# Kernel tuning notes

Measured on AMD Instinct MI355X. Metric: run time of the kernel, lower is better.

## Reference

```python
import jax, jax.numpy as jnp
import numpy as np

BATCH = 512          # bs_large + bs_small
COMBINED_BS = 320    # bs_large + bs_small // (r_large // r_small)
R = 64               # r_large
K = 4096             # hidden dim, fixed in the TIR kernel
N_ADAPT = 80         # combined adapters


def setup_inputs() -> dict:
    key = jax.random.key(0)
    k1, k2, k3, k4 = jax.random.split(key, 4)
    x = jax.random.normal(k1, (BATCH, 1, K), dtype=jnp.float32)
    xids = jax.random.randint(k2, (COMBINED_BS * R,), 0, BATCH, dtype=jnp.int32)
    wids = jax.random.randint(k3, (COMBINED_BS,), 0, N_ADAPT, dtype=jnp.int32)
    A = jax.random.normal(k4, (N_ADAPT, K, R), dtype=jnp.float32) * 0.02
    return {"x": x, "xids": xids, "wids": wids, "A": A}


def reference(x, xids, wids, A):
    # out[c, 0, r] = sum_k x[xids[c*R + r], 0, k] * A[wids[c], k, r]
    C = wids.shape[0]
    r = A.shape[2]
    tok = xids.reshape(C, r)          # per-output-element token ids
    xg = x[tok, 0, :]                 # (C, R, K) gathered activations
    Ag = A[wids]                      # (C, K, R) gathered adapters
    out = jnp.einsum('crk,ckr->cr', xg, Ag)
    return out[:, None, :]            # (C, 1, R)
```

## Files before the change

kernel.cpp:

```cpp
#include <hip/hip_runtime.h>
#include <stdint.h>

namespace {
constexpr int BATCH  = 512;
constexpr int CBS    = 320;
constexpr int R      = 64;
constexpr int K      = 4096;
constexpr int NADAPT = 80;
constexpr int SPLIT  = 8;
constexpr int KS     = K / SPLIT;
constexpr int TK     = 64;
constexpr int NT     = 256;
constexpr int NW     = NT / 64;
constexpr int NTILES = KS / TK;

constexpr size_t WS_X_OFF  = 4096;
constexpr size_t WS_NEEDED = WS_X_OFF + (size_t)BATCH * K * 2;

__device__ inline uint16_t f2bf(float f) {
    uint32_t u = __float_as_uint(f);
    u += 0x7fffu + ((u >> 16) & 1u);
    return (uint16_t)(u >> 16);
}
__device__ inline float bf2f(uint16_t b) {
    return __uint_as_float((uint32_t)b << 16);
}
}

__global__ void sort_by_wid(const int* __restrict__ wids, int* __restrict__ perm)
{
    __shared__ int hist[NADAPT];
    __shared__ int offs[NADAPT];
    const int t = threadIdx.x;
    if (t < NADAPT) hist[t] = 0;
    __syncthreads();
    atomicAdd(&hist[wids[t]], 1);
    __syncthreads();
    if (t == 0) {
        int run = 0;
        for (int i = 0; i < NADAPT; ++i) { offs[i] = run; run += hist[i]; }
    }
    __syncthreads();
    const int pos = atomicAdd(&offs[wids[t]], 1);
    perm[pos] = t;
}

__global__ __launch_bounds__(256)
void cvt_x(const float* __restrict__ x, uint16_t* __restrict__ xb)
{
    const int i = blockIdx.x * 256 + threadIdx.x;
    const float4 v = ((const float4*)x)[i];
    ushort4 o;
    o.x = f2bf(v.x); o.y = f2bf(v.y); o.z = f2bf(v.z); o.w = f2bf(v.w);
    ((ushort4*)xb)[i] = o;
}

__global__ __launch_bounds__(NT)
void lora_main(const int* __restrict__ xids,
               const int* __restrict__ wids,
               const float* __restrict__ A,
               const uint16_t* __restrict__ xb,
               const int* __restrict__ perm,
               float* __restrict__ out)
{
    __shared__ float xs[TK * R];
    __shared__ float red[NW * R];

    const int bid  = blockIdx.x;
    const int i0   = bid >> 3;
    const int s    = bid & 7;
    const int c    = perm[i0];
    const int t    = threadIdx.x;
    const int wave = t >> 6;
    const int lane = t & 63;
    const int r4   = lane & 15;
    const int kq   = lane >> 4;

    const int wid = wids[c];
    const float* __restrict__ Aw = A + (size_t)wid * (K * R);

    const int rw  = t >> 2;
    const int jq  = t & 3;
    const int tok = xids[c * R + rw];
    const uint16_t* __restrict__ xrow = xb + (size_t)tok * K + s * KS + jq * 16;
    const int rsw = rw ^ (jq * 16);

    float4 acc = make_float4(0.f, 0.f, 0.f, 0.f);

    uint4 p0, p1;
    {
        const uint4* src = (const uint4*)xrow;
        p0 = src[0]; p1 = src[1];
    }

    for (int tile = 0; tile < NTILES; ++tile) {
        {
            const uint32_t w[8] = {p0.x, p0.y, p0.z, p0.w, p1.x, p1.y, p1.z, p1.w};
            float* base = xs + (jq * 16) * R + rsw;
#pragma unroll
            for (int m = 0; m < 8; ++m) {
                base[(2 * m + 0) * R] = bf2f((uint16_t)(w[m] & 0xffffu));
                base[(2 * m + 1) * R] = bf2f((uint16_t)(w[m] >> 16));
            }
        }
        __syncthreads();

        if (tile + 1 < NTILES) {
            const uint4* src = (const uint4*)(xrow + (tile + 1) * TK);
            p0 = src[0]; p1 = src[1];
        }

        const int kw = wave * 16 + kq;
        const int rr = (4 * r4) ^ (wave * 16);
        const float* __restrict__ Ap =
            Aw + (size_t)(s * KS + tile * TK + kw) * R + 4 * r4;
#pragma unroll
        for (int i = 0; i < 4; ++i) {
            float4 av = *(const float4*)(Ap + (size_t)(4 * i) * R);
            float4 xv = *(const float4*)(&xs[(kw + 4 * i) * R + rr]);
            acc.x = fmaf(xv.x, av.x, acc.x);
            acc.y = fmaf(xv.y, av.y, acc.y);
            acc.z = fmaf(xv.z, av.z, acc.z);
            acc.w = fmaf(xv.w, av.w, acc.w);
        }
        __syncthreads();
    }

#pragma unroll
    for (int m = 16; m < 64; m <<= 1) {
        acc.x += __shfl_xor(acc.x, m, 64);
        acc.y += __shfl_xor(acc.y, m, 64);
        acc.z += __shfl_xor(acc.z, m, 64);
        acc.w += __shfl_xor(acc.w, m, 64);
    }
    if (kq == 0) {
        float* rd = &red[wave * R + 4 * r4];
        rd[0] = acc.x; rd[1] = acc.y; rd[2] = acc.z; rd[3] = acc.w;
    }
    __syncthreads();
    if (wave == 0) {
        float sum = red[lane] + red[R + lane] + red[2 * R + lane] + red[3 * R + lane];
        atomicAdd(&out[c * R + lane], sum);
    }
}

__global__ __launch_bounds__(NT)
void lora_fallback(const float* __restrict__ x,
                   const int*   __restrict__ xids,
                   const int*   __restrict__ wids,
                   const float* __restrict__ A,
                   float*       __restrict__ out)
{
    __shared__ float xs[TK * R];
    __shared__ float red[NW * R];
    const int bid  = blockIdx.x;
    const int c    = bid >> 3;
    const int s    = bid & 7;
    const int t    = threadIdx.x;
    const int wave = t >> 6;
    const int lane = t & 63;
    const int r4   = lane & 15;
    const int kq   = lane >> 4;
    const int wid  = wids[c];
    const float* __restrict__ Aw = A + (size_t)wid * (K * R);
    const int rw  = t >> 2;
    const int jq  = t & 3;
    const int tok = xids[c * R + rw];
    const float* __restrict__ xrow = x + (size_t)tok * K + s * KS + jq * 16;
    float4 acc = make_float4(0.f, 0.f, 0.f, 0.f);
    float4 pv[4];
    {
        const float4* src = (const float4*)xrow;
#pragma unroll
        for (int ii = 0; ii < 4; ++ii) pv[ii] = src[ii];
    }
    for (int tile = 0; tile < NTILES; ++tile) {
#pragma unroll
        for (int ii = 0; ii < 4; ++ii) {
            const int kk = jq * 16 + ii * 4;
            xs[(kk + 0) * R + rw] = pv[ii].x;
            xs[(kk + 1) * R + rw] = pv[ii].y;
            xs[(kk + 2) * R + rw] = pv[ii].z;
            xs[(kk + 3) * R + rw] = pv[ii].w;
        }
        __syncthreads();
        if (tile + 1 < NTILES) {
            const float4* src = (const float4*)(xrow + (tile + 1) * TK);
#pragma unroll
            for (int ii = 0; ii < 4; ++ii) pv[ii] = src[ii];
        }
        const int kw = wave * 16 + kq;
        const float* __restrict__ Ap =
            Aw + (size_t)(s * KS + tile * TK + kw) * R + 4 * r4;
#pragma unroll
        for (int i = 0; i < 4; ++i) {
            float4 av = *(const float4*)(Ap + (size_t)(4 * i) * R);
            float4 xv = *(const float4*)(&xs[(kw + 4 * i) * R + 4 * r4]);
            acc.x = fmaf(xv.x, av.x, acc.x);
            acc.y = fmaf(xv.y, av.y, acc.y);
            acc.z = fmaf(xv.z, av.z, acc.z);
            acc.w = fmaf(xv.w, av.w, acc.w);
        }
        __syncthreads();
    }
#pragma unroll
    for (int m = 16; m < 64; m <<= 1) {
        acc.x += __shfl_xor(acc.x, m, 64);
        acc.y += __shfl_xor(acc.y, m, 64);
        acc.z += __shfl_xor(acc.z, m, 64);
        acc.w += __shfl_xor(acc.w, m, 64);
    }
    if (kq == 0) {
        float* rd = &red[wave * R + 4 * r4];
        rd[0] = acc.x; rd[1] = acc.y; rd[2] = acc.z; rd[3] = acc.w;
    }
    __syncthreads();
    if (wave == 0) {
        float sum = red[lane] + red[R + lane] + red[2 * R + lane] + red[3 * R + lane];
        atomicAdd(&out[c * R + lane], sum);
    }
}

extern "C" void kernel_launch(void* const* d_in, const int* in_sizes, int n_in,
                              void* d_out, int out_size, void* d_ws, size_t ws_size,
                              hipStream_t stream)
{
    (void)in_sizes; (void)n_in;
    const float* x    = (const float*)d_in[0];
    const int*   xids = (const int*)d_in[1];
    const int*   wids = (const int*)d_in[2];
    const float* A    = (const float*)d_in[3];
    float* out        = (float*)d_out;

    hipMemsetAsync(out, 0, (size_t)out_size * sizeof(float), stream);

    if (ws_size >= WS_NEEDED) {
        int*      perm = (int*)d_ws;
        uint16_t* xb   = (uint16_t*)((char*)d_ws + WS_X_OFF);
        hipLaunchKernelGGL(sort_by_wid, dim3(1), dim3(CBS), 0, stream, wids, perm);
        hipLaunchKernelGGL(cvt_x, dim3(BATCH * K / 4 / 256), dim3(256), 0, stream, x, xb);
        hipLaunchKernelGGL(lora_main, dim3(CBS * SPLIT), dim3(NT), 0, stream,
                           xids, wids, A, xb, perm, out);
    } else {
        hipLaunchKernelGGL(lora_fallback, dim3(CBS * SPLIT), dim3(NT), 0, stream,
                           x, xids, wids, A, out);
    }
}
```

Baseline: 147.7 us.

## Group up to four same-adapter rows per block to reuse adapter tile loads

Rows that share an adapter id are bucketed into groups of up to four. Each block now loads one A tile and applies it to up to four gathered activation rows, so A traffic per output row drops. Activations stay packed as bf16 pairs in shared memory and are unpacked at use time. Grid size is now an upper bound on the group count, with empty groups exiting early. In exchange the kernel uses more shared memory and registers per block, and the register prefetch of the next x tile is removed.

```diff
diff --git a/kernel.cpp b/kernel.cpp
--- a/kernel.cpp
+++ b/kernel.cpp
@@ -13,36 +13,45 @@
 constexpr int NT     = 256;
 constexpr int NW     = NT / 64;
 constexpr int NTILES = KS / TK;
-
-constexpr size_t WS_X_OFF  = 4096;
-constexpr size_t WS_NEEDED = WS_X_OFF + (size_t)BATCH * K * 2;
+constexpr int G      = 4;
+constexpr int MAXG   = (CBS + (G - 1) * NADAPT) / G;
+
+constexpr size_t WS_XB_OFF = 8192;
+constexpr size_t WS_NEEDED = WS_XB_OFF + (size_t)BATCH * K * 2;
 
 __device__ inline uint16_t f2bf(float f) {
     uint32_t u = __float_as_uint(f);
     u += 0x7fffu + ((u >> 16) & 1u);
     return (uint16_t)(u >> 16);
 }
-__device__ inline float bf2f(uint16_t b) {
-    return __uint_as_float((uint32_t)b << 16);
-}
-}
-
-__global__ void sort_by_wid(const int* __restrict__ wids, int* __restrict__ perm)
+__device__ inline float bflo(uint32_t u) { return __uint_as_float(u << 16); }
+__device__ inline float bfhi(uint32_t u) { return __uint_as_float(u & 0xffff0000u); }
+}
+
+__global__ void groups_build(const int* __restrict__ wids,
+                             int* __restrict__ gcnt, int* __restrict__ gwid,
+                             int* __restrict__ gc)
 {
     __shared__ int hist[NADAPT];
     __shared__ int offs[NADAPT];
+    __shared__ int gbase[NADAPT];
     const int t = threadIdx.x;
-    if (t < NADAPT) hist[t] = 0;
+    if (t < NADAPT) { hist[t] = 0; offs[t] = 0; }
+    if (t < MAXG) gcnt[t] = 0;
     __syncthreads();
     atomicAdd(&hist[wids[t]], 1);
     __syncthreads();
     if (t == 0) {
         int run = 0;
-        for (int i = 0; i < NADAPT; ++i) { offs[i] = run; run += hist[i]; }
-    }
-    __syncthreads();
-    const int pos = atomicAdd(&offs[wids[t]], 1);
-    perm[pos] = t;
+        for (int w = 0; w < NADAPT; ++w) { gbase[w] = run; run += (hist[w] + G - 1) / G; }
+    }
+    __syncthreads();
+    const int w   = wids[t];
+    const int rk  = atomicAdd(&offs[w], 1);
+    const int gid = gbase[w] + (rk >> 2);
+    gc[gid * G + (rk & 3)] = t;
+    gwid[gid] = w;
+    atomicAdd(&gcnt[gid], 1);
 }
 
 __global__ __launch_bounds__(256)
@@ -57,90 +66,119 @@
 
 __global__ __launch_bounds__(NT)
 void lora_main(const int* __restrict__ xids,
-               const int* __restrict__ wids,
                const float* __restrict__ A,
                const uint16_t* __restrict__ xb,
-               const int* __restrict__ perm,
+               const int* __restrict__ gcnt, const int* __restrict__ gwid,
+               const int* __restrict__ gc,
                float* __restrict__ out)
 {
-    __shared__ float xs[TK * R];
-    __shared__ float red[NW * R];
-
-    const int bid  = blockIdx.x;
-    const int i0   = bid >> 3;
-    const int s    = bid & 7;
-    const int c    = perm[i0];
+    __shared__ uint32_t xs[G * (TK / 2) * R];
+    __shared__ float red[G * NW * R];
+
+    const int bid = blockIdx.x;
+    const int gid = bid >> 3;
+    const int s   = bid & 7;
+    const int cnt = gcnt[gid];
+    if (cnt == 0) return;
+    const int wid = gwid[gid];
+    const float* __restrict__ Aw = A + (size_t)wid * (K * R);
+
     const int t    = threadIdx.x;
     const int wave = t >> 6;
     const int lane = t & 63;
     const int r4   = lane & 15;
     const int kq   = lane >> 4;
-
-    const int wid = wids[c];
-    const float* __restrict__ Aw = A + (size_t)wid * (K * R);
-
-    const int rw  = t >> 2;
-    const int jq  = t & 3;
-    const int tok = xids[c * R + rw];
-    const uint16_t* __restrict__ xrow = xb + (size_t)tok * K + s * KS + jq * 16;
-    const int rsw = rw ^ (jq * 16);
-
-    float4 acc = make_float4(0.f, 0.f, 0.f, 0.f);
-
-    uint4 p0, p1;
+    const int rw   = t >> 2;
+    const int jq   = t & 3;
+    const int rsw  = rw ^ (jq << 4);
+
+    const uint16_t* __restrict__ xrow[G];
+#pragma unroll
+    for (int g = 0; g < G; ++g) {
+        const int c   = (g < cnt) ? gc[gid * G + g] : 0;
+        const int tok = xids[c * R + rw];
+        xrow[g] = xb + (size_t)tok * K + s * KS + jq * 16;
+    }
+
+    float4 acc[G];
+#pragma unroll
+    for (int g = 0; g < G; ++g) acc[g] = make_float4(0.f, 0.f, 0.f, 0.f);
+
+    const int wsw = wave << 4;
+    const int p1  = wave * 8 + kq;
+    const int rr  = (4 * r4) ^ wsw;
+
+    for (int tile = 0; tile < NTILES; ++tile) {
+#pragma unroll
+        for (int g = 0; g < G; ++g) {
+            if (g < cnt) {
+                const uint4* src = (const uint4*)(xrow[g] + tile * TK);
+                uint4 u0 = src[0], u1 = src[1];
+                uint32_t* dst = &xs[g * 2048 + (jq * 8) * R + rsw];
+                dst[0 * R] = u0.x; dst[1 * R] = u0.y; dst[2 * R] = u0.z; dst[3 * R] = u0.w;
+                dst[4 * R] = u1.x; dst[5 * R] = u1.y; dst[6 * R] = u1.z; dst[7 * R] = u1.w;
+            }
+        }
+        __syncthreads();
+
+        const int k0 = s * KS + tile * TK + wave * 16 + 2 * kq;
+        const float* __restrict__ Ap = Aw + (size_t)k0 * R + 4 * r4;
+        const float4 a0 = *(const float4*)(Ap);
+        const float4 a1 = *(const float4*)(Ap + R);
+        const float4 a2 = *(const float4*)(Ap + 8 * R);
+        const float4 a3 = *(const float4*)(Ap + 9 * R);
+
+#pragma unroll
+        for (int g = 0; g < G; ++g) {
+            if (g < cnt) {
+                const uint32_t* b = &xs[g * 2048];
+                const uint4 f1 = *(const uint4*)&b[p1 * R + rr];
+                const uint4 f2 = *(const uint4*)&b[(p1 + 4) * R + rr];
+                acc[g].x = fmaf(bflo(f1.x), a0.x, acc[g].x);
+                acc[g].y = fmaf(bflo(f1.y), a0.y, acc[g].y);
+                acc[g].z = fmaf(bflo(f1.z), a0.z, acc[g].z);
+                acc[g].w = fmaf(bflo(f1.w), a0.w, acc[g].w);
+                acc[g].x = fmaf(bfhi(f1.x), a1.x, acc[g].x);
+                acc[g].y = fmaf(bfhi(f1.y), a1.y, acc[g].y);
+                acc[g].z = fmaf(bfhi(f1.z), a1.z, acc[g].z);
+                acc[g].w = fmaf(bfhi(f1.w), a1.w, acc[g].w);
+                acc[g].x = fmaf(bflo(f2.x), a2.x, acc[g].x);
+                acc[g].y = fmaf(bflo(f2.y), a2.y, acc[g].y);
+                acc[g].z = fmaf(bflo(f2.z), a2.z, acc[g].z);
+                acc[g].w = fmaf(bflo(f2.w), a2.w, acc[g].w);
+                acc[g].x = fmaf(bfhi(f2.x), a3.x, acc[g].x);
+                acc[g].y = fmaf(bfhi(f2.y), a3.y, acc[g].y);
+                acc[g].z = fmaf(bfhi(f2.z), a3.z, acc[g].z);
+                acc[g].w = fmaf(bfhi(f2.w), a3.w, acc[g].w);
+            }
+        }
+        __syncthreads();
+    }
+
+#pragma unroll
+    for (int g = 0; g < G; ++g) {
+#pragma unroll
+        for (int m = 16; m < 64; m <<= 1) {
+            acc[g].x += __shfl_xor(acc[g].x, m, 64);
+            acc[g].y += __shfl_xor(acc[g].y, m, 64);
+            acc[g].z += __shfl_xor(acc[g].z, m, 64);
+            acc[g].w += __shfl_xor(acc[g].w, m, 64);
+        }
+    }
+    if (kq == 0) {
+#pragma unroll
+        for (int g = 0; g < G; ++g)
+            *(float4*)&red[(g * NW + wave) * R + 4 * r4] = acc[g];
+    }
+    __syncthreads();
     {
-        const uint4* src = (const uint4*)xrow;
-        p0 = src[0]; p1 = src[1];
-    }
-
-    for (int tile = 0; tile < NTILES; ++tile) {
-        {
-            const uint32_t w[8] = {p0.x, p0.y, p0.z, p0.w, p1.x, p1.y, p1.z, p1.w};
-            float* base = xs + (jq * 16) * R + rsw;
-#pragma unroll
-            for (int m = 0; m < 8; ++m) {
-                base[(2 * m + 0) * R] = bf2f((uint16_t)(w[m] & 0xffffu));
-                base[(2 * m + 1) * R] = bf2f((uint16_t)(w[m] >> 16));
-            }
-        }
-        __syncthreads();
-
-        if (tile + 1 < NTILES) {
-            const uint4* src = (const uint4*)(xrow + (tile + 1) * TK);
-            p0 = src[0]; p1 = src[1];
-        }
-
-        const int kw = wave * 16 + kq;
-        const int rr = (4 * r4) ^ (wave * 16);
-        const float* __restrict__ Ap =
-            Aw + (size_t)(s * KS + tile * TK + kw) * R + 4 * r4;
-#pragma unroll
-        for (int i = 0; i < 4; ++i) {
-            float4 av = *(const float4*)(Ap + (size_t)(4 * i) * R);
-            float4 xv = *(const float4*)(&xs[(kw + 4 * i) * R + rr]);
-            acc.x = fmaf(xv.x, av.x, acc.x);
-            acc.y = fmaf(xv.y, av.y, acc.y);
-            acc.z = fmaf(xv.z, av.z, acc.z);
-            acc.w = fmaf(xv.w, av.w, acc.w);
-        }
-        __syncthreads();
-    }
-
-#pragma unroll
-    for (int m = 16; m < 64; m <<= 1) {
-        acc.x += __shfl_xor(acc.x, m, 64);
-        acc.y += __shfl_xor(acc.y, m, 64);
-        acc.z += __shfl_xor(acc.z, m, 64);
-        acc.w += __shfl_xor(acc.w, m, 64);
-    }
-    if (kq == 0) {
-        float* rd = &red[wave * R + 4 * r4];
-        rd[0] = acc.x; rd[1] = acc.y; rd[2] = acc.z; rd[3] = acc.w;
-    }
-    __syncthreads();
-    if (wave == 0) {
-        float sum = red[lane] + red[R + lane] + red[2 * R + lane] + red[3 * R + lane];
-        atomicAdd(&out[c * R + lane], sum);
+        const int g = wave;
+        if (g < cnt) {
+            const int c = gc[gid * G + g];
+            const float sum = red[(g * NW + 0) * R + lane] + red[(g * NW + 1) * R + lane]
+                            + red[(g * NW + 2) * R + lane] + red[(g * NW + 3) * R + lane];
+            atomicAdd(&out[c * R + lane], sum);
+        }
     }
 }
 
@@ -151,7 +189,7 @@
                    const float* __restrict__ A,
                    float*       __restrict__ out)
 {
-    __shared__ float xs[TK * R];
+    __shared__ float xsf[TK * R];
     __shared__ float red[NW * R];
     const int bid  = blockIdx.x;
     const int c    = bid >> 3;
@@ -168,34 +206,25 @@
     const int tok = xids[c * R + rw];
     const float* __restrict__ xrow = x + (size_t)tok * K + s * KS + jq * 16;
     float4 acc = make_float4(0.f, 0.f, 0.f, 0.f);
-    float4 pv[4];
-    {
-        const float4* src = (const float4*)xrow;
-#pragma unroll
-        for (int ii = 0; ii < 4; ++ii) pv[ii] = src[ii];
-    }
     for (int tile = 0; tile < NTILES; ++tile) {
+        const float4* src = (const float4*)(xrow + tile * TK);
 #pragma unroll
         for (int ii = 0; ii < 4; ++ii) {
+            float4 v = src[ii];
             const int kk = jq * 16 + ii * 4;
-            xs[(kk + 0) * R + rw] = pv[ii].x;
-            xs[(kk + 1) * R + rw] = pv[ii].y;
-            xs[(kk + 2) * R + rw] = pv[ii].z;
-            xs[(kk + 3) * R + rw] = pv[ii].w;
-        }
-        __syncthreads();
-        if (tile + 1 < NTILES) {
-            const float4* src = (const float4*)(xrow + (tile + 1) * TK);
-#pragma unroll
-            for (int ii = 0; ii < 4; ++ii) pv[ii] = src[ii];
-        }
+            xsf[(kk + 0) * R + rw] = v.x;
+            xsf[(kk + 1) * R + rw] = v.y;
+            xsf[(kk + 2) * R + rw] = v.z;
+            xsf[(kk + 3) * R + rw] = v.w;
+        }
+        __syncthreads();
         const int kw = wave * 16 + kq;
         const float* __restrict__ Ap =
             Aw + (size_t)(s * KS + tile * TK + kw) * R + 4 * r4;
 #pragma unroll
         for (int i = 0; i < 4; ++i) {
             float4 av = *(const float4*)(Ap + (size_t)(4 * i) * R);
-            float4 xv = *(const float4*)(&xs[(kw + 4 * i) * R + 4 * r4]);
+            float4 xv = *(const float4*)(&xsf[(kw + 4 * i) * R + 4 * r4]);
             acc.x = fmaf(xv.x, av.x, acc.x);
             acc.y = fmaf(xv.y, av.y, acc.y);
             acc.z = fmaf(xv.z, av.z, acc.z);
@@ -235,12 +264,16 @@
     hipMemsetAsync(out, 0, (size_t)out_size * sizeof(float), stream);
 
     if (ws_size >= WS_NEEDED) {
-        int*      perm = (int*)d_ws;
-        uint16_t* xb   = (uint16_t*)((char*)d_ws + WS_X_OFF);
-        hipLaunchKernelGGL(sort_by_wid, dim3(1), dim3(CBS), 0, stream, wids, perm);
+        int*      wsi  = (int*)d_ws;
+        int*      gcnt = wsi;
+        int*      gwid = wsi + 256;
+        int*      gc   = wsi + 512;
+        uint16_t* xb   = (uint16_t*)((char*)d_ws + WS_XB_OFF);
+        hipLaunchKernelGGL(groups_build, dim3(1), dim3(CBS), 0, stream,
+                           wids, gcnt, gwid, gc);
         hipLaunchKernelGGL(cvt_x, dim3(BATCH * K / 4 / 256), dim3(256), 0, stream, x, xb);
-        hipLaunchKernelGGL(lora_main, dim3(CBS * SPLIT), dim3(NT), 0, stream,
-                           xids, wids, A, xb, perm, out);
+        hipLaunchKernelGGL(lora_main, dim3(MAXG * SPLIT), dim3(NT), 0, stream,
+                           xids, A, xb, gcnt, gwid, gc, out);
     } else {
         hipLaunchKernelGGL(lora_fallback, dim3(CBS * SPLIT), dim3(NT), 0, stream,
                            x, xids, wids, A, out);
```

After: 149.7 us. Within noise of the previous version (+1.4%).
